# Performance work log

Measured on AMD Instinct MI355X. Metric: run time of the kernel, lower is better.

## Reference

```python
import jax, jax.numpy as jnp
import numpy as np

KS = 4                                  # kernel_size per axis
K = KS ** 3                             # 64 spatial filter bins
RADIUS = np.float32(1.5 * 6 * 0.025 / 2.0)   # filter_extent / 2 = 0.1125
N_REAL = 20000                          # fluid particles (index N_REAL = far dummy)
E_PAD = 1200000                         # padded edge count


def ball_to_cube(u):
    # volume-preserving unit-ball -> [-1,1]^3 cube map (Griepentrog et al., as in
    # Open3D-ML 'ball_to_cube_volume_preserving'): ball -> cylinder -> cube.
    eps = 1e-9
    x, y, z = u[..., 0], u[..., 1], u[..., 2]
    sq = x * x + y * y + z * z
    norm = jnp.sqrt(sq + eps)
    rxy2 = x * x + y * y
    polar = 1.25 * z * z > rxy2          # top/bottom cone region
    s = jnp.where(polar,
                  jnp.sqrt(3.0 * norm / (norm + jnp.abs(z) + eps)),
                  norm / jnp.sqrt(rxy2 + eps))
    xc = x * s
    yc = y * s
    zc = jnp.where(polar, jnp.sign(z) * norm, 1.5 * z)
    degen = sq < 1e-12
    xc = jnp.where(degen, 0.0, xc)
    yc = jnp.where(degen, 0.0, yc)
    zc = jnp.where(degen, 0.0, zc)
    # cylinder -> cube: inverse concentric (Shirley-Chiu) area-preserving map on xy
    r = jnp.sqrt(xc * xc + yc * yc + eps)
    c1 = jnp.abs(xc) >= jnp.abs(yc)
    xs = jnp.where(jnp.abs(xc) < eps, eps, xc)
    ys = jnp.where(jnp.abs(yc) < eps, eps, yc)
    fop = np.float32(4.0 / np.pi)
    a = jnp.where(c1, jnp.sign(xc) * r, jnp.sign(yc) * r * fop * jnp.arctan(xc / ys))
    b = jnp.where(c1, jnp.sign(xc) * r * fop * jnp.arctan(yc / xs), jnp.sign(yc) * r)
    tiny = (xc * xc + yc * yc) < 1e-12
    a = jnp.where(tiny, 0.0, a)
    b = jnp.where(tiny, 0.0, b)
    return jnp.stack([a, b, zc], axis=-1)


def cconv(feat, pos, src, dst, W, b):
    # ContinuousConv: normalize=False, align_corners=True, linear interpolation,
    # poly6 window on r^2/radius^2, self-neighbors excluded in the edge list.
    offs = (pos[dst] - pos[src]) / RADIUS              # (E,3), inside unit ball
    r2 = jnp.sum(offs * offs, axis=-1)
    win = jnp.clip((1.0 - r2) ** 3, 0.0, 1.0)          # window_poly6; 0 on pad edges
    g = jnp.clip((ball_to_cube(offs) * 0.5 + 0.5) * (KS - 1), 0.0, KS - 1)
    f0f = jnp.floor(g)
    t = g - f0f                                         # trilinear fractions
    f0 = f0f.astype(jnp.int32)
    fj = feat[dst] * win[:, None]                       # (E,Cin) windowed neighbor feats
    n = pos.shape[0]
    cin = feat.shape[1]
    B = jnp.zeros((n * K, cin), feat.dtype)             # per-query per-bin accumulator
    for c in range(8):                                  # 8 trilinear corners
        w = jnp.ones_like(r2)
        kf = jnp.zeros_like(src)
        for ax in range(3):
            bit = (c >> (2 - ax)) & 1
            ia = jnp.minimum(f0[:, ax] + bit, KS - 1)
            w = w * (t[:, ax] if bit else 1.0 - t[:, ax])
            kf = kf * KS + ia
        B = B + jax.ops.segment_sum(fj * w[:, None], src * K + kf, num_segments=n * K)
    out = jnp.einsum('nki,kio->no', B.reshape(n, K, cin), W.reshape(K, cin, -1))
    return out + b


def forward(pos, feats, edge_src, edge_dst, conv0_w, conv0_b, dense0_w, dense0_b,
            conv1_w, conv1_b, dense1_w, dense1_b, conv2_w, conv2_b, dense2_w, dense2_b,
            conv3_w, conv3_b, dense3_w, dense3_b):
    f = jnp.concatenate([jnp.ones_like(pos[:, :1]), feats], axis=-1)   # 13 channels
    x = jnp.concatenate([cconv(f, pos, edge_src, edge_dst, conv0_w, conv0_b),
                         f @ dense0_w + dense0_b], axis=-1)            # 64 + 32 = 96
    layers = [(conv1_w, conv1_b, dense1_w, dense1_b),
              (conv2_w, conv2_b, dense2_w, dense2_b),
              (conv3_w, conv3_b, dense3_w, dense3_b)]
    for cw, cb, dw, db in layers:
        inp = jax.nn.relu(x)
        y = cconv(inp, pos, edge_src, edge_dst, cw, cb) + inp @ dw + db
        x = (y + x) if y.shape[-1] == x.shape[-1] else y               # residual 64->64
    return (x * (1.0 / 128.0))[:N_REAL]                                # pos_correction


def setup_inputs() -> dict:
    rng = np.random.default_rng(0)
    spacing = 0.05                                  # 2 * particle_radius
    g = np.arange(28)
    pts = np.stack(np.meshgrid(g, g, g, indexing='ij'), -1).reshape(-1, 3).astype(np.float64) * spacing
    pts = pts[:N_REAL] + rng.uniform(-0.012, 0.012, (N_REAL, 3))
    # fixed-radius neighbor search, excluding self (radius_search_ignore_query_points)
    r2 = float(RADIUS) ** 2
    sq = (pts ** 2).sum(-1)
    src_l, dst_l = [], []
    for s in range(0, N_REAL, 1000):
        q = pts[s:s + 1000]
        d2 = (q ** 2).sum(-1)[:, None] + sq[None, :] - 2.0 * (q @ pts.T)
        ii, jj = np.nonzero(d2 < r2)
        ii = ii + s
        keep = ii != jj
        src_l.append(ii[keep])
        dst_l.append(jj[keep])
    src = np.concatenate(src_l).astype(np.int32)[:E_PAD]
    dst = np.concatenate(dst_l).astype(np.int32)[:E_PAD]
    pad = E_PAD - src.size
    src = np.concatenate([src, np.zeros(pad, np.int32)])
    dst = np.concatenate([dst, np.full(pad, N_REAL, np.int32)])   # edges to far dummy -> window 0
    pos = np.concatenate([pts, [[1e3, 1e3, 1e3]]], 0).astype(np.float32)
    key = jax.random.key(0)
    ks = jax.random.split(key, 12)
    def w(k, shape, fan_in):
        return jax.random.normal(k, shape, jnp.float32) * np.float32(1.0 / np.sqrt(fan_in))
    return {
        'pos': jnp.asarray(pos),
        'feats': jax.random.normal(ks[0], (N_REAL + 1, 12), jnp.float32),
        'edge_src': jnp.asarray(src),
        'edge_dst': jnp.asarray(dst),
        'conv0_w': w(ks[1], (KS, KS, KS, 13, 64), 13 * 27),
        'conv0_b': jnp.zeros((64,), jnp.float32),
        'dense0_w': w(ks[2], (13, 32), 13),
        'dense0_b': jnp.zeros((32,), jnp.float32),
        'conv1_w': w(ks[3], (KS, KS, KS, 96, 64), 96 * 27),
        'conv1_b': jnp.zeros((64,), jnp.float32),
        'dense1_w': w(ks[4], (96, 64), 96),
        'dense1_b': jnp.zeros((64,), jnp.float32),
        'conv2_w': w(ks[5], (KS, KS, KS, 64, 64), 64 * 27),
        'conv2_b': jnp.zeros((64,), jnp.float32),
        'dense2_w': w(ks[6], (64, 64), 64),
        'dense2_b': jnp.zeros((64,), jnp.float32),
        'conv3_w': w(ks[7], (KS, KS, KS, 64, 3), 64 * 27),
        'conv3_b': jnp.zeros((3,), jnp.float32),
        'dense3_w': w(ks[8], (64, 3), 64),
        'dense3_b': jnp.zeros((3,), jnp.float32),
    }


def reference(pos, feats, edge_src, edge_dst, conv0_w, conv0_b, dense0_w, dense0_b,
              conv1_w, conv1_b, dense1_w, dense1_b, conv2_w, conv2_b, dense2_w, dense2_b,
              conv3_w, conv3_b, dense3_w, dense3_b):
    return forward(pos, feats, edge_src, edge_dst, conv0_w, conv0_b, dense0_w, dense0_b,
                   conv1_w, conv1_b, dense1_w, dense1_b, conv2_w, conv2_b, dense2_w, dense2_b,
                   conv3_w, conv3_b, dense3_w, dense3_b)
```

## Files before the change

kernel.cpp:

```cpp
#include <hip/hip_runtime.h>
#include <math.h>

#define NPTS   20001
#define NREAL  20000
#define EPAD   1200000
#define KK     64
#define RADF   0.1125f

typedef _Float16 half8_t __attribute__((ext_vector_type(8)));
typedef float    floatx4 __attribute__((ext_vector_type(4)));

__device__ __forceinline__ float sgnf(float v){ return v>0.f ? 1.f : (v<0.f ? -1.f : 0.f); }
__device__ __forceinline__ _Float16 lo16(unsigned u){ return __builtin_bit_cast(_Float16, (unsigned short)(u & 0xffffu)); }
__device__ __forceinline__ _Float16 hi16(unsigned u){ return __builtin_bit_cast(_Float16, (unsigned short)(u >> 16)); }

__device__ __forceinline__ void* swzp(void* base, int byteoff){
  return (void*)((char*)base + (byteoff ^ (((byteoff >> 6) & 7) << 4)));
}
__device__ __forceinline__ const void* swzp(const void* base, int byteoff){
  return (const void*)((const char*)base + (byteoff ^ (((byteoff >> 6) & 7) << 4)));
}

__global__ void k_find_ereal(const int* __restrict__ dst, int* __restrict__ ereal){
  int lo=0, hi=EPAD;
  while(lo<hi){ int mid=(lo+hi)>>1; if(dst[mid]==NREAL) hi=mid; else lo=mid+1; }
  *ereal = lo;
}

__global__ void k_csr(const int* __restrict__ src, const int* __restrict__ erealp,
                      int* __restrict__ row_start){
  int i = blockIdx.x*blockDim.x + threadIdx.x;
  if(i > NPTS) return;
  int E = *erealp;
  int lo=0, hi=E;
  while(lo<hi){ int mid=(lo+hi)>>1; if(src[mid] < i) lo=mid+1; else hi=mid; }
  row_start[i] = lo;
}

__global__ void k_build_f(const float* __restrict__ feats, float* __restrict__ f){
  int idx = blockIdx.x*blockDim.x + threadIdx.x;
  if(idx >= NPTS*13) return;
  int i = idx/13, c = idx - i*13;
  f[idx] = (c==0) ? 1.f : feats[i*12 + (c-1)];
}

__global__ void k_cvtF(const float* __restrict__ x, unsigned* __restrict__ Fp, int total){
  int idx = blockIdx.x*blockDim.x + threadIdx.x;
  if(idx >= total) return;
  float v = fmaxf(x[idx], 0.f);
  _Float16 h = (_Float16)v;
  _Float16 l = (_Float16)(v - (float)h);
  Fp[idx] = (unsigned)__builtin_bit_cast(unsigned short, h)
          | ((unsigned)__builtin_bit_cast(unsigned short, l) << 16);
}

__device__ __forceinline__ void edge_geom(float ox, float oy, float oz,
                                          float& win, float& t0, float& t1, float& t2, int& f0p){
  const float eps = 1e-9f;
  float sq = ox*ox + oy*oy + oz*oz;
  float u = 1.f - sq;
  win = fminf(fmaxf(u*u*u, 0.f), 1.f);
  float norm = sqrtf(sq + eps);
  float rxy2 = ox*ox + oy*oy;
  bool polar = (1.25f*oz*oz > rxy2);
  float s_p = sqrtf(3.f*norm/(norm + fabsf(oz) + eps));
  float s_n = norm / sqrtf(rxy2 + eps);
  float s = polar ? s_p : s_n;
  float xc = ox*s, yc = oy*s;
  float zc = polar ? sgnf(oz)*norm : 1.5f*oz;
  if(sq < 1e-12f){ xc = 0.f; yc = 0.f; zc = 0.f; }
  float r = sqrtf(xc*xc + yc*yc + eps);
  bool c1 = fabsf(xc) >= fabsf(yc);
  float xs = (fabsf(xc) < eps) ? eps : xc;
  float ys = (fabsf(yc) < eps) ? eps : yc;
  const float fop = 1.2732395447351628f;
  float a = c1 ? sgnf(xc)*r : sgnf(yc)*r*fop*atanf(xc/ys);
  float b = c1 ? sgnf(xc)*r*fop*atanf(yc/xs) : sgnf(yc)*r;
  if(xc*xc + yc*yc < 1e-12f){ a = 0.f; b = 0.f; }
  float g0 = fminf(fmaxf((a *0.5f+0.5f)*3.f, 0.f), 3.f);
  float g1 = fminf(fmaxf((b *0.5f+0.5f)*3.f, 0.f), 3.f);
  float g2 = fminf(fmaxf((zc*0.5f+0.5f)*3.f, 0.f), 3.f);
  float f00 = floorf(g0), f01 = floorf(g1), f02 = floorf(g2);
  t0 = g0 - f00; t1 = g1 - f01; t2 = g2 - f02;
  f0p = (int)f00 | ((int)f01 << 2) | ((int)f02 << 4);
}

__global__ __launch_bounds__(256) void k_geom(const float* __restrict__ pos,
    const int* __restrict__ esrc, const int* __restrict__ edst,
    float4* __restrict__ gw, int4* __restrict__ gmz)
{
  int e = blockIdx.x*blockDim.x + threadIdx.x;
  if(e >= EPAD) return;
  const int sn = esrc[e], d = edst[e];
  const float ox = (pos[d*3+0]-pos[sn*3+0])/RADF;
  const float oy = (pos[d*3+1]-pos[sn*3+1])/RADF;
  const float oz = (pos[d*3+2]-pos[sn*3+2])/RADF;
  float win, t0, t1, t2; int f0p;
  edge_geom(ox, oy, oz, win, t0, t1, t2, f0p);
  const int i0 = f0p & 3, i1 = (f0p>>2) & 3, i2 = f0p >> 4;
  const int X0 = i0 << 4, X1 = ((i0+1)&3) << 4;
  const int Y0 = i1 << 2, Y1 = ((i1+1)&3) << 2;
  const int Z0 = i2, Z1 = (i2+1) & 3;
  const float wx0 = win*(1.f-t0), wx1 = win*t0;
  const float wy0 = 1.f-t1, wy1 = t1;
  const float wz0 = 1.f-t2, wz1 = t2;
  gw[e] = make_float4(wx0*wy0, wx0*wy1, wx1*wy0, wx1*wy1);
  const int p0 = Z0 & 1;
  const float zA = p0 ? wz1 : wz0;
  const int   cA = p0 ? Z1 : Z0;
  const int   cB = p0 ? Z0 : Z1;
  const int cells0 = (X0|Y0|cA) | ((X0|Y1|cA)<<8) | ((X1|Y0|cA)<<16) | ((X1|Y1|cA)<<24);
  const int cells1 = (X0|Y0|cB) | ((X0|Y1|cB)<<8) | ((X1|Y0|cB)<<16) | ((X1|Y1|cB)<<24);
  gmz[e] = make_int4(__float_as_int(zA), cells0, cells1, d);
}

template<int OUT3>
__global__ __launch_bounds__(256) void k_scat64m(
    const unsigned* __restrict__ Fp, const float4* __restrict__ gw,
    const int4* __restrict__ gmz, const int* __restrict__ row_start,
    float* __restrict__ B, int node_base,
    const float* __restrict__ W3, float* __restrict__ out)
{
  __shared__ __align__(128) _Float16 Wh[64*32];
  __shared__ __align__(128) _Float16 Wl[64*32];
  __shared__ __align__(128) _Float16 Fh[64*32];
  __shared__ __align__(128) _Float16 Fl[64*32];
  __shared__ __align__(16) float4 Sq[32];
  __shared__ __align__(16) int4   Smd[32];
  __shared__ float red[16];

  const int tid  = threadIdx.x;
  const int node = node_base + blockIdx.x;
  const int wv   = tid >> 6;
  const int lane = tid & 63;
  const int frow = lane & 15;
  const int fb   = (lane >> 4) << 4;

  floatx4 acc[4];
  #pragma unroll
  for(int nt=0;nt<4;++nt){ acc[nt][0]=0.f; acc[nt][1]=0.f; acc[nt][2]=0.f; acc[nt][3]=0.f; }

  half8_t hz;
  #pragma unroll
  for(int q8=0;q8<8;++q8) hz[q8] = (_Float16)0;

  const int e0 = row_start[node], e1 = row_start[node+1];

  for(int eb = e0; eb < e1; eb += 32){
    const int n = (e1 - eb < 32) ? (e1 - eb) : 32;
    __syncthreads();
    if(wv == 0){
      if(lane < 32){
        int ei = eb + lane; if(ei >= e1) ei = e1 - 1;
        Sq[lane]  = gw[ei];
        Smd[lane] = gmz[ei];
      }
    } else {
      for(int j = tid - 64; j < 512; j += 192){
        if(j < 256) ((half8_t*)Wh)[j]       = hz;
        else        ((half8_t*)Wl)[j - 256] = hz;
      }
    }
    __syncthreads();
    {
      half8_t hreg, lreg;
      #pragma unroll
      for(int j=0;j<8;++j){
        const int dst = Smd[wv*8 + j].w;
        const unsigned u = Fp[(size_t)dst*64 + lane];
        hreg[j] = lo16(u);
        lreg[j] = hi16(u);
      }
      *(half8_t*)swzp(Fh, (lane<<6) + (wv<<4)) = hreg;
      *(half8_t*)swzp(Fl, (lane<<6) + (wv<<4)) = lreg;
    }
    if(lane < 8){
      const int ei = wv*8 + lane;
      if(ei < n){
        const float4 q  = Sq[ei];
        const int4   md = Smd[ei];
        const float zA = __int_as_float(md.x), zB = 1.f - zA;
        #pragma unroll
        for(int t=0;t<8;++t){
          const int   cells = (t < 4) ? md.y : md.z;
          const float zz    = (t < 4) ? zA : zB;
          const int   cell  = (cells >> ((t & 3) * 8)) & 255;
          const float qq    = ((t&3)==0) ? q.x : ((t&3)==1) ? q.y : ((t&3)==2) ? q.z : q.w;
          const float wgt   = qq * zz;
          const _Float16 h  = (_Float16)wgt;
          *(_Float16*)swzp(Wh, (cell<<6) + (ei<<1)) = h;
          *(_Float16*)swzp(Wl, (cell<<6) + (ei<<1)) = (_Float16)(wgt - (float)h);
        }
      }
    }
    __syncthreads();
    const half8_t ah = *(const half8_t*)swzp(Wh, ((wv*16 + frow)<<6) + fb);
    const half8_t al = *(const half8_t*)swzp(Wl, ((wv*16 + frow)<<6) + fb);
    #pragma unroll
    for(int nt=0; nt<4; ++nt){
      const half8_t bh = *(const half8_t*)swzp(Fh, ((nt*16 + frow)<<6) + fb);
      const half8_t bl = *(const half8_t*)swzp(Fl, ((nt*16 + frow)<<6) + fb);
      acc[nt] = __builtin_amdgcn_mfma_f32_16x16x32_f16(ah, bh, acc[nt], 0, 0, 0);
      acc[nt] = __builtin_amdgcn_mfma_f32_16x16x32_f16(al, bh, acc[nt], 0, 0, 0);
      acc[nt] = __builtin_amdgcn_mfma_f32_16x16x32_f16(ah, bl, acc[nt], 0, 0, 0);
    }
  }

  if(!OUT3){
    float* Bg = B + (size_t)blockIdx.x*4096;
    #pragma unroll
    for(int nt=0;nt<4;++nt)
      #pragma unroll
      for(int r=0;r<4;++r){
        const int cell = wv*16 + (lane>>4)*4 + r;
        Bg[cell*64 + nt*16 + (lane&15)] = acc[nt][r];
      }
  } else {
    float s0=0.f, s1=0.f, s2=0.f;
    #pragma unroll
    for(int nt=0;nt<4;++nt){
      #pragma unroll
      for(int r=0;r<4;++r){
        const int cell = wv*16 + (lane>>4)*4 + r;
        const int j3   = (cell*64 + nt*16 + (lane&15)) * 3;
        const float v  = acc[nt][r];
        s0 = fmaf(v, W3[j3+0], s0);
        s1 = fmaf(v, W3[j3+1], s1);
        s2 = fmaf(v, W3[j3+2], s2);
      }
    }
    #pragma unroll
    for(int off = 32; off > 0; off >>= 1){
      s0 += __shfl_down(s0, off);
      s1 += __shfl_down(s1, off);
      s2 += __shfl_down(s2, off);
    }
    if(lane == 0){
      red[wv*4+0] = s0; red[wv*4+1] = s1; red[wv*4+2] = s2;
    }
    __syncthreads();
    if(tid == 0 && node < NREAL){
      out[node*3+0] += (red[0]+red[4]+red[8] +red[12])*(1.f/128.f);
      out[node*3+1] += (red[1]+red[5]+red[9] +red[13])*(1.f/128.f);
      out[node*3+2] += (red[2]+red[6]+red[10]+red[14])*(1.f/128.f);
    }
  }
}

__global__ __launch_bounds__(256) void k_scat96m(
    const unsigned* __restrict__ Fp, const float4* __restrict__ gw,
    const int4* __restrict__ gmz, const int* __restrict__ row_start,
    float* __restrict__ B, int node_base)
{
  __shared__ __align__(128) _Float16 Wh[64*32];
  __shared__ __align__(128) _Float16 Wl[64*32];
  __shared__ __align__(128) _Float16 Fh[96*32];
  __shared__ __align__(128) _Float16 Fl[96*32];
  __shared__ __align__(16) float4 Sq[32];
  __shared__ __align__(16) int4   Smd[32];

  const int tid  = threadIdx.x;
  const int node = node_base + blockIdx.x;
  const int wv   = tid >> 6;
  const int lane = tid & 63;
  const int frow = lane & 15;
  const int fb   = (lane >> 4) << 4;

  floatx4 acc[6];
  #pragma unroll
  for(int nt=0;nt<6;++nt){ acc[nt][0]=0.f; acc[nt][1]=0.f; acc[nt][2]=0.f; acc[nt][3]=0.f; }

  half8_t hz;
  #pragma unroll
  for(int q8=0;q8<8;++q8) hz[q8] = (_Float16)0;

  const int e0 = row_start[node], e1 = row_start[node+1];

  for(int eb = e0; eb < e1; eb += 32){
    const int n = (e1 - eb < 32) ? (e1 - eb) : 32;
    __syncthreads();
    if(wv == 0){
      if(lane < 32){
        int ei = eb + lane; if(ei >= e1) ei = e1 - 1;
        Sq[lane]  = gw[ei];
        Smd[lane] = gmz[ei];
      }
    } else {
      for(int j = tid - 64; j < 512; j += 192){
        if(j < 256) ((half8_t*)Wh)[j]       = hz;
        else        ((half8_t*)Wl)[j - 256] = hz;
      }
    }
    __syncthreads();
    {
      half8_t h0, l0, h1, l1;
      #pragma unroll
      for(int j=0;j<8;++j){
        const int dst = Smd[wv*8 + j].w;
        const unsigned u = Fp[(size_t)dst*96 + lane];
        h0[j] = lo16(u);
        l0[j] = hi16(u);
        if(lane < 32){
          const unsigned u2 = Fp[(size_t)dst*96 + 64 + lane];
          h1[j] = lo16(u2);
          l1[j] = hi16(u2);
        }
      }
      *(half8_t*)swzp(Fh, (lane<<6) + (wv<<4)) = h0;
      *(half8_t*)swzp(Fl, (lane<<6) + (wv<<4)) = l0;
      if(lane < 32){
        *(half8_t*)swzp(Fh, ((64+lane)<<6) + (wv<<4)) = h1;
        *(half8_t*)swzp(Fl, ((64+lane)<<6) + (wv<<4)) = l1;
      }
    }
    if(lane < 8){
      const int ei = wv*8 + lane;
      if(ei < n){
        const float4 q  = Sq[ei];
        const int4   md = Smd[ei];
        const float zA = __int_as_float(md.x), zB = 1.f - zA;
        #pragma unroll
        for(int t=0;t<8;++t){
          const int   cells = (t < 4) ? md.y : md.z;
          const float zz    = (t < 4) ? zA : zB;
          const int   cell  = (cells >> ((t & 3) * 8)) & 255;
          const float qq    = ((t&3)==0) ? q.x : ((t&3)==1) ? q.y : ((t&3)==2) ? q.z : q.w;
          const float wgt   = qq * zz;
          const _Float16 h  = (_Float16)wgt;
          *(_Float16*)swzp(Wh, (cell<<6) + (ei<<1)) = h;
          *(_Float16*)swzp(Wl, (cell<<6) + (ei<<1)) = (_Float16)(wgt - (float)h);
        }
      }
    }
    __syncthreads();
    const half8_t ah = *(const half8_t*)swzp(Wh, ((wv*16 + frow)<<6) + fb);
    const half8_t al = *(const half8_t*)swzp(Wl, ((wv*16 + frow)<<6) + fb);
    #pragma unroll
    for(int nt=0; nt<6; ++nt){
      const half8_t bh = *(const half8_t*)swzp(Fh, ((nt*16 + frow)<<6) + fb);
      const half8_t bl = *(const half8_t*)swzp(Fl, ((nt*16 + frow)<<6) + fb);
      acc[nt] = __builtin_amdgcn_mfma_f32_16x16x32_f16(ah, bh, acc[nt], 0, 0, 0);
      acc[nt] = __builtin_amdgcn_mfma_f32_16x16x32_f16(al, bh, acc[nt], 0, 0, 0);
      acc[nt] = __builtin_amdgcn_mfma_f32_16x16x32_f16(ah, bl, acc[nt], 0, 0, 0);
    }
  }

  float* Bg = B + (size_t)blockIdx.x*6144;
  #pragma unroll
  for(int nt=0;nt<6;++nt)
    #pragma unroll
    for(int r=0;r<4;++r){
      const int cell = wv*16 + (lane>>4)*4 + r;
      Bg[cell*96 + nt*16 + (lane&15)] = acc[nt][r];
    }
}

__global__ __launch_bounds__(128) void k_scat13(
    const float* __restrict__ feat, const float4* __restrict__ gw,
    const int4* __restrict__ gmz, const int* __restrict__ row_start,
    float* __restrict__ B, int node_base)
{
  constexpr int CIN = 13, BSZ = KK*CIN, ESW = 4, CSTRIDE = BSZ + 8;
  __shared__ __align__(16) float Bl[ESW*CSTRIDE];
  const int tid  = threadIdx.x;
  const int node = node_base + blockIdx.x;

  for(int j = tid; j < ESW*CSTRIDE; j += 128) Bl[j] = 0.f;

  const int e0 = row_start[node], e1 = row_start[node+1];
  const int wv   = tid >> 6;
  const int lane = tid & 63;
  const int slot = lane >> 4;
  const int c    = lane & 15;
  const bool act = (c < CIN);
  float* Bp = Bl + slot*CSTRIDE;
  __syncthreads();

  if(act){
    for(int e = e0 + slot; e < e1; e += ESW){
      const float4 q  = gw[e];
      const int4   md = gmz[e];
      const float zA = __int_as_float(md.x);
      const float z  = wv ? (1.f - zA) : zA;
      const int   cp = wv ? md.z : md.y;
      float v = feat[(size_t)md.w*CIN + c] * z;
      const int b0 = ( cp        & 255)*CIN + c;
      const int b1 = ((cp >> 8)  & 255)*CIN + c;
      const int b2 = ((cp >> 16) & 255)*CIN + c;
      const int b3 = (((unsigned)cp) >> 24)*CIN + c;
      float o0 = Bp[b0], o1 = Bp[b1], o2 = Bp[b2], o3 = Bp[b3];
      o0 = fmaf(q.x, v, o0); o1 = fmaf(q.y, v, o1);
      o2 = fmaf(q.z, v, o2); o3 = fmaf(q.w, v, o3);
      Bp[b0] = o0; Bp[b1] = o1; Bp[b2] = o2; Bp[b3] = o3;
    }
  }
  __syncthreads();

  float* Bg = B + (size_t)blockIdx.x*BSZ;
  for(int j = tid*4; j < BSZ; j += 512){
    float4 a = *(const float4*)&Bl[j];
    #pragma unroll
    for(int k = 1; k < ESW; ++k){
      const float4 t = *(const float4*)&Bl[k*CSTRIDE + j];
      a.x += t.x; a.y += t.y; a.z += t.z; a.w += t.w;
    }
    *(float4*)&Bg[j] = a;
  }
}

__global__ void k_cvtW(const float* __restrict__ W, _Float16* __restrict__ WhT,
                       _Float16* __restrict__ WlT, int Kd)
{
  int idx = blockIdx.x*blockDim.x + threadIdx.x;
  if(idx >= 64*Kd) return;
  int o = idx / Kd, k = idx - o*Kd;
  float w = W[(size_t)k*64 + o];
  _Float16 h = (_Float16)w;
  WhT[idx] = h;
  WlT[idx] = (_Float16)(w - (float)h);
}

__global__ __launch_bounds__(256) void k_gemm_mfma(
    const float* __restrict__ A, const _Float16* __restrict__ WhT,
    const _Float16* __restrict__ WlT, float* __restrict__ P,
    int M, int Kd, int node_base, int ksteps_per)
{
  __shared__ __align__(128) _Float16 Ah[64*32];
  __shared__ __align__(128) _Float16 Al[64*32];
  __shared__ __align__(128) _Float16 Bh[64*32];
  __shared__ __align__(128) _Float16 Blo[64*32];
  const int tid = threadIdx.x;
  const int mbase = blockIdx.x * 64;
  const int s = blockIdx.y;
  const int kt0 = s * ksteps_per * 32;
  const int kt1 = min(Kd, kt0 + ksteps_per*32);
  const int wv = tid >> 6, lane = tid & 63;
  const int row  = tid >> 2;
  const int kseg = (tid & 3) * 8;
  const int sb   = (tid & 3) << 4;
  const int frow = lane & 15;
  const int fb   = (lane >> 4) << 4;

  floatx4 acc[4];
  #pragma unroll
  for(int c=0;c<4;++c){ acc[c][0]=0.f; acc[c][1]=0.f; acc[c][2]=0.f; acc[c][3]=0.f; }

  const int grow = mbase + row;
  const float* Arow = (grow < M) ? (A + (size_t)grow*Kd) : nullptr;
  const _Float16* WhRow = WhT + (size_t)row*Kd;
  const _Float16* WlRow = WlT + (size_t)row*Kd;

  for(int kt = kt0; kt < kt1; kt += 32){
    float av[8];
    if(Arow){
      *(float4*)&av[0] = *(const float4*)(Arow + kt + kseg);
      *(float4*)&av[4] = *(const float4*)(Arow + kt + kseg + 4);
    } else {
      #pragma unroll
      for(int j=0;j<8;++j) av[j] = 0.f;
    }
    half8_t hv, lv;
    #pragma unroll
    for(int j=0;j<8;++j){
      _Float16 h = (_Float16)av[j];
      hv[j] = h;
      lv[j] = (_Float16)(av[j] - (float)h);
    }
    half8_t wh = *(const half8_t*)(WhRow + kt + kseg);
    half8_t wl = *(const half8_t*)(WlRow + kt + kseg);
    __syncthreads();
    *(half8_t*)swzp(Ah,  (row<<6) + sb) = hv;
    *(half8_t*)swzp(Al,  (row<<6) + sb) = lv;
    *(half8_t*)swzp(Bh,  (row<<6) + sb) = wh;
    *(half8_t*)swzp(Blo, (row<<6) + sb) = wl;
    __syncthreads();
    const half8_t ah = *(const half8_t*)swzp(Ah, ((wv*16 + frow)<<6) + fb);
    const half8_t al = *(const half8_t*)swzp(Al, ((wv*16 + frow)<<6) + fb);
    #pragma unroll
    for(int c=0;c<4;++c){
      const half8_t bh = *(const half8_t*)swzp(Bh,  ((c*16 + frow)<<6) + fb);
      const half8_t bl = *(const half8_t*)swzp(Blo, ((c*16 + frow)<<6) + fb);
      acc[c] = __builtin_amdgcn_mfma_f32_16x16x32_f16(ah, bh, acc[c], 0, 0, 0);
      acc[c] = __builtin_amdgcn_mfma_f32_16x16x32_f16(al, bh, acc[c], 0, 0, 0);
      acc[c] = __builtin_amdgcn_mfma_f32_16x16x32_f16(ah, bl, acc[c], 0, 0, 0);
    }
  }

  const int prow0 = mbase + wv*16 + (lane>>4)*4;
  const int pcol  = lane & 15;
  #pragma unroll
  for(int c=0;c<4;++c){
    #pragma unroll
    for(int r=0;r<4;++r){
      const int rr = prow0 + r;
      if(rr < M)
        P[((size_t)s*NPTS + node_base + rr)*64 + c*16 + pcol] = acc[c][r];
    }
  }
}

template<int S>
__global__ void k_combine(const float* __restrict__ P, float* __restrict__ x,
                          int ldout, int colofs)
{
  int idx = blockIdx.x*blockDim.x + threadIdx.x;
  if(idx >= NPTS*16) return;
  int node = idx >> 4, c4 = (idx & 15) * 4;
  float4 s = *(const float4*)(P + (size_t)node*64 + c4);
  #pragma unroll
  for(int k=1;k<S;++k){
    float4 t = *(const float4*)(P + ((size_t)k*NPTS + node)*64 + c4);
    s.x+=t.x; s.y+=t.y; s.z+=t.z; s.w+=t.w;
  }
  float* xp = x + (size_t)node*ldout + colofs + c4;
  float4 o = *(float4*)xp;
  o.x+=s.x; o.y+=s.y; o.z+=s.z; o.w+=s.w;
  *(float4*)xp = o;
}

__global__ void k_dense0(const float* __restrict__ f, const float* __restrict__ dW,
                         const float* __restrict__ db, const float* __restrict__ cb0,
                         float* __restrict__ out)
{
  int idx = blockIdx.x*blockDim.x + threadIdx.x;
  if(idx >= NPTS*96) return;
  int i = idx/96, c = idx - i*96;
  if(c < 64){ out[idx] = cb0[c]; return; }
  int o = c - 64;
  float s = db[o];
  const float* row = f + (size_t)i*13;
  #pragma unroll
  for(int j=0;j<13;++j) s = fmaf(row[j], dW[j*32+o], s);
  out[idx] = s;
}

__global__ void k_dense(const float* __restrict__ in, int cin,
                        const float* __restrict__ dW, const float* __restrict__ db,
                        const float* __restrict__ cb, const float* __restrict__ resid,
                        float* __restrict__ out)
{
  int idx = blockIdx.x*blockDim.x + threadIdx.x;
  if(idx >= NPTS*64) return;
  int i = idx >> 6, o = idx & 63;
  float s = db[o] + cb[o];
  if(resid) s += resid[idx];
  const float* row = in + (size_t)i*cin;
  for(int c=0;c<cin;++c) s = fmaf(fmaxf(row[c],0.f), dW[c*64+o], s);
  out[idx] = s;
}

__global__ void k_dense3(const float* __restrict__ x2, const float* __restrict__ dW,
                         const float* __restrict__ db, const float* __restrict__ cb,
                         float* __restrict__ out)
{
  int idx = blockIdx.x*blockDim.x + threadIdx.x;
  if(idx >= NREAL*3) return;
  int i = idx/3, o = idx - i*3;
  float s = db[o] + cb[o];
  const float* row = x2 + (size_t)i*64;
  for(int c=0;c<64;++c) s = fmaf(fmaxf(row[c],0.f), dW[c*3+o], s);
  out[idx] = s * (1.f/128.f);
}

static inline size_t alup(size_t x){ return (x + 255) & ~(size_t)255; }

static inline int calc_rows(size_t bcap, int cin, int want){
  size_t perrow = (size_t)KK * cin * 4;
  size_t r = (perrow > 0) ? bcap / perrow : 0;
  if(r >= (size_t)want) return want;
  r = (r / 128) * 128;
  if(r < 128) r = 128;
  return (int)r;
}

extern "C" void kernel_launch(void* const* d_in, const int* in_sizes, int n_in,
                              void* d_out, int out_size, void* d_ws, size_t ws_size,
                              hipStream_t stream)
{
  const float* pos   = (const float*)d_in[0];
  const float* feats = (const float*)d_in[1];
  const int*   esrc  = (const int*)d_in[2];
  const int*   edst  = (const int*)d_in[3];
  const float* c0w = (const float*)d_in[4];
  const float* c0b = (const float*)d_in[5];
  const float* d0w = (const float*)d_in[6];
  const float* d0b = (const float*)d_in[7];
  const float* c1w = (const float*)d_in[8];
  const float* c1b = (const float*)d_in[9];
  const float* d1w = (const float*)d_in[10];
  const float* d1b = (const float*)d_in[11];
  const float* c2w = (const float*)d_in[12];
  const float* c2b = (const float*)d_in[13];
  const float* d2w = (const float*)d_in[14];
  const float* d2b = (const float*)d_in[15];
  const float* c3w = (const float*)d_in[16];
  const float* c3b = (const float*)d_in[17];
  const float* d3w = (const float*)d_in[18];
  const float* d3b = (const float*)d_in[19];
  float* out = (float*)d_out;

  char* w = (char*)d_ws;
  size_t off = 0;
  float* f  = (float*)(w+off); off += alup((size_t)NPTS*13*4);
  float* x0 = (float*)(w+off); off += alup((size_t)NPTS*96*4);
  float* x1 = (float*)(w+off); off += alup((size_t)NPTS*64*4);
  float* x2 = (float*)(w+off); off += alup((size_t)NPTS*64*4);
  int* row_start = (int*)(w+off); off += alup((size_t)(NPTS+1)*4);
  int* ereal = (int*)(w+off);     off += alup(16);
  float4* gw = (float4*)(w+off);  off += alup((size_t)EPAD*16);
  int4*  gmz = (int4*)(w+off);    off += alup((size_t)EPAD*16);
  float* P  = (float*)(w+off); off += alup((size_t)8*NPTS*64*4);
  _Float16* whT = (_Float16*)(w+off); off += alup((size_t)64*6144*2);
  _Float16* wlT = (_Float16*)(w+off); off += alup((size_t)64*6144*2);
  unsigned* Fp0 = (unsigned*)(w+off); off += alup((size_t)NPTS*96*4);
  unsigned* Fp1 = (unsigned*)(w+off); off += alup((size_t)NPTS*64*4);
  float* B = (float*)(w+off);
  size_t bcap = (ws_size > off) ? (ws_size - off) : 0;

  k_find_ereal<<<1,1,0,stream>>>(edst, ereal);
  k_csr<<<(NPTS+1+255)/256,256,0,stream>>>(esrc, ereal, row_start);
  k_build_f<<<(NPTS*13+255)/256,256,0,stream>>>(feats, f);
  k_geom<<<(EPAD+255)/256,256,0,stream>>>(pos, esrc, edst, gw, gmz);

  k_dense0<<<(NPTS*96+255)/256,256,0,stream>>>(f, d0w, d0b, c0b, x0);
  {
    k_cvtW<<<(64*832+255)/256,256,0,stream>>>(c0w, whT, wlT, 832);
    int rows = calc_rows(bcap, 13, 8192);
    for(int base = 0; base < NPTS; base += rows){
      int m = (NPTS - base < rows) ? (NPTS - base) : rows;
      k_scat13<<<m,128,0,stream>>>(f, gw, gmz, row_start, B, base);
      k_gemm_mfma<<<dim3((m+63)/64, 8),256,0,stream>>>(B, whT, wlT, P, m, 832, base, 4);
    }
    k_combine<8><<<(NPTS*16+255)/256,256,0,stream>>>(P, x0, 96, 0);
  }

  k_dense<<<(NPTS*64+255)/256,256,0,stream>>>(x0, 96, d1w, d1b, c1b, nullptr, x1);
  {
    k_cvtW<<<(64*6144+255)/256,256,0,stream>>>(c1w, whT, wlT, 6144);
    k_cvtF<<<(NPTS*96+255)/256,256,0,stream>>>(x0, Fp0, NPTS*96);
    int rows = calc_rows(bcap, 96, 4096);
    for(int base = 0; base < NPTS; base += rows){
      int m = (NPTS - base < rows) ? (NPTS - base) : rows;
      k_scat96m<<<m,256,0,stream>>>(Fp0, gw, gmz, row_start, B, base);
      k_gemm_mfma<<<dim3((m+63)/64, 8),256,0,stream>>>(B, whT, wlT, P, m, 6144, base, 24);
    }
    k_combine<8><<<(NPTS*16+255)/256,256,0,stream>>>(P, x1, 64, 0);
  }

  k_dense<<<(NPTS*64+255)/256,256,0,stream>>>(x1, 64, d2w, d2b, c2b, x1, x2);
  {
    k_cvtW<<<(64*4096+255)/256,256,0,stream>>>(c2w, whT, wlT, 4096);
    k_cvtF<<<(NPTS*64+255)/256,256,0,stream>>>(x1, Fp1, NPTS*64);
    int rows = calc_rows(bcap, 64, 4096);
    for(int base = 0; base < NPTS; base += rows){
      int m = (NPTS - base < rows) ? (NPTS - base) : rows;
      k_scat64m<0><<<m,256,0,stream>>>(Fp1, gw, gmz, row_start, B, base, nullptr, nullptr);
      k_gemm_mfma<<<dim3((m+63)/64, 8),256,0,stream>>>(B, whT, wlT, P, m, 4096, base, 16);
    }
    k_combine<8><<<(NPTS*16+255)/256,256,0,stream>>>(P, x2, 64, 0);
  }

  k_dense3<<<(NREAL*3+255)/256,256,0,stream>>>(x2, d3w, d3b, c3b, out);
  k_cvtF<<<(NPTS*64+255)/256,256,0,stream>>>(x2, Fp1, NPTS*64);
  k_scat64m<1><<<NPTS,256,0,stream>>>(Fp1, gw, gmz, row_start, nullptr, 0, c3w, out);
}
```

Before: 968.5 us.

## Pre-split scatter output into packed fp16 hi/lo and enlarge GEMM M-tile

The scatter kernels now write their per-node basis matrix B as packed fp16 hi/lo pairs instead of fp32, so the GEMM no longer does the split-conversion per tile. The GEMM block tile grows from 64 to 128 rows, with each wave computing two 16-row tiles, so every weight tile loaded into shared memory is reused across twice as many rows. B traffic stays the same size (4 bytes per element) but conversion work moves to the producer. The larger tile halves the grid in M and raises register use from the accumulators, which may lower occupancy.

```diff
diff --git a/kernel.cpp b/kernel.cpp
--- a/kernel.cpp
+++ b/kernel.cpp
@@ -13,6 +13,12 @@
 __device__ __forceinline__ float sgnf(float v){ return v>0.f ? 1.f : (v<0.f ? -1.f : 0.f); }
 __device__ __forceinline__ _Float16 lo16(unsigned u){ return __builtin_bit_cast(_Float16, (unsigned short)(u & 0xffffu)); }
 __device__ __forceinline__ _Float16 hi16(unsigned u){ return __builtin_bit_cast(_Float16, (unsigned short)(u >> 16)); }
+__device__ __forceinline__ unsigned packf(float v){
+  _Float16 h = (_Float16)v;
+  _Float16 l = (_Float16)(v - (float)h);
+  return (unsigned)__builtin_bit_cast(unsigned short, h)
+       | ((unsigned)__builtin_bit_cast(unsigned short, l) << 16);
+}
 
 __device__ __forceinline__ void* swzp(void* base, int byteoff){
   return (void*)((char*)base + (byteoff ^ (((byteoff >> 6) & 7) << 4)));
@@ -47,11 +53,7 @@
 __global__ void k_cvtF(const float* __restrict__ x, unsigned* __restrict__ Fp, int total){
   int idx = blockIdx.x*blockDim.x + threadIdx.x;
   if(idx >= total) return;
-  float v = fmaxf(x[idx], 0.f);
-  _Float16 h = (_Float16)v;
-  _Float16 l = (_Float16)(v - (float)h);
-  Fp[idx] = (unsigned)__builtin_bit_cast(unsigned short, h)
-          | ((unsigned)__builtin_bit_cast(unsigned short, l) << 16);
+  Fp[idx] = packf(fmaxf(x[idx], 0.f));
 }
 
 __device__ __forceinline__ void edge_geom(float ox, float oy, float oz,
@@ -118,7 +120,7 @@
 __global__ __launch_bounds__(256) void k_scat64m(
     const unsigned* __restrict__ Fp, const float4* __restrict__ gw,
     const int4* __restrict__ gmz, const int* __restrict__ row_start,
-    float* __restrict__ B, int node_base,
+    unsigned* __restrict__ B, int node_base,
     const float* __restrict__ W3, float* __restrict__ out)
 {
   __shared__ __align__(128) _Float16 Wh[64*32];
@@ -207,13 +209,13 @@
   }
 
   if(!OUT3){
-    float* Bg = B + (size_t)blockIdx.x*4096;
+    unsigned* Bg = B + (size_t)blockIdx.x*4096;
     #pragma unroll
     for(int nt=0;nt<4;++nt)
       #pragma unroll
       for(int r=0;r<4;++r){
         const int cell = wv*16 + (lane>>4)*4 + r;
-        Bg[cell*64 + nt*16 + (lane&15)] = acc[nt][r];
+        Bg[cell*64 + nt*16 + (lane&15)] = packf(acc[nt][r]);
       }
   } else {
     float s0=0.f, s1=0.f, s2=0.f;
@@ -250,7 +252,7 @@
 __global__ __launch_bounds__(256) void k_scat96m(
     const unsigned* __restrict__ Fp, const float4* __restrict__ gw,
     const int4* __restrict__ gmz, const int* __restrict__ row_start,
-    float* __restrict__ B, int node_base)
+    unsigned* __restrict__ B, int node_base)
 {
   __shared__ __align__(128) _Float16 Wh[64*32];
   __shared__ __align__(128) _Float16 Wl[64*32];
@@ -345,20 +347,20 @@
     }
   }
 
-  float* Bg = B + (size_t)blockIdx.x*6144;
+  unsigned* Bg = B + (size_t)blockIdx.x*6144;
   #pragma unroll
   for(int nt=0;nt<6;++nt)
     #pragma unroll
     for(int r=0;r<4;++r){
       const int cell = wv*16 + (lane>>4)*4 + r;
-      Bg[cell*96 + nt*16 + (lane&15)] = acc[nt][r];
+      Bg[cell*96 + nt*16 + (lane&15)] = packf(acc[nt][r]);
     }
 }
 
 __global__ __launch_bounds__(128) void k_scat13(
     const float* __restrict__ feat, const float4* __restrict__ gw,
     const int4* __restrict__ gmz, const int* __restrict__ row_start,
-    float* __restrict__ B, int node_base)
+    unsigned* __restrict__ B, int node_base)
 {
   constexpr int CIN = 13, BSZ = KK*CIN, ESW = 4, CSTRIDE = BSZ + 8;
   __shared__ __align__(16) float Bl[ESW*CSTRIDE];
@@ -396,7 +398,7 @@
   }
   __syncthreads();
 
-  float* Bg = B + (size_t)blockIdx.x*BSZ;
+  unsigned* Bg = B + (size_t)blockIdx.x*BSZ;
   for(int j = tid*4; j < BSZ; j += 512){
     float4 a = *(const float4*)&Bl[j];
     #pragma unroll
@@ -404,7 +406,9 @@
       const float4 t = *(const float4*)&Bl[k*CSTRIDE + j];
       a.x += t.x; a.y += t.y; a.z += t.z; a.w += t.w;
     }
-    *(float4*)&Bg[j] = a;
+    uint4 o;
+    o.x = packf(a.x); o.y = packf(a.y); o.z = packf(a.z); o.w = packf(a.w);
+    *(uint4*)&Bg[j] = o;
   }
 }
 
@@ -421,80 +425,100 @@
 }
 
 __global__ __launch_bounds__(256) void k_gemm_mfma(
-    const float* __restrict__ A, const _Float16* __restrict__ WhT,
+    const unsigned* __restrict__ Ap, const _Float16* __restrict__ WhT,
     const _Float16* __restrict__ WlT, float* __restrict__ P,
     int M, int Kd, int node_base, int ksteps_per)
 {
-  __shared__ __align__(128) _Float16 Ah[64*32];
-  __shared__ __align__(128) _Float16 Al[64*32];
+  __shared__ __align__(128) _Float16 Ah[128*32];
+  __shared__ __align__(128) _Float16 Al[128*32];
   __shared__ __align__(128) _Float16 Bh[64*32];
   __shared__ __align__(128) _Float16 Blo[64*32];
   const int tid = threadIdx.x;
-  const int mbase = blockIdx.x * 64;
+  const int mbase = blockIdx.x * 128;
   const int s = blockIdx.y;
   const int kt0 = s * ksteps_per * 32;
   const int kt1 = min(Kd, kt0 + ksteps_per*32);
   const int wv = tid >> 6, lane = tid & 63;
-  const int row  = tid >> 2;
-  const int kseg = (tid & 3) * 8;
-  const int sb   = (tid & 3) << 4;
+  const int arow = tid >> 1;
+  const int aseg = (tid & 1) * 16;
+  const int wrow = tid >> 2;
+  const int wseg = (tid & 3) * 8;
   const int frow = lane & 15;
   const int fb   = (lane >> 4) << 4;
 
-  floatx4 acc[4];
-  #pragma unroll
-  for(int c=0;c<4;++c){ acc[c][0]=0.f; acc[c][1]=0.f; acc[c][2]=0.f; acc[c][3]=0.f; }
-
-  const int grow = mbase + row;
-  const float* Arow = (grow < M) ? (A + (size_t)grow*Kd) : nullptr;
-  const _Float16* WhRow = WhT + (size_t)row*Kd;
-  const _Float16* WlRow = WlT + (size_t)row*Kd;
+  floatx4 acc[2][4];
+  #pragma unroll
+  for(int rt=0;rt<2;++rt)
+    #pragma unroll
+    for(int c=0;c<4;++c){ acc[rt][c][0]=0.f; acc[rt][c][1]=0.f; acc[rt][c][2]=0.f; acc[rt][c][3]=0.f; }
+
+  const int grow = mbase + arow;
+  const unsigned* Arow = (grow < M) ? (Ap + (size_t)grow*Kd) : nullptr;
+  const _Float16* WhRow = WhT + (size_t)wrow*Kd;
+  const _Float16* WlRow = WlT + (size_t)wrow*Kd;
 
   for(int kt = kt0; kt < kt1; kt += 32){
-    float av[8];
+    unsigned au[16];
     if(Arow){
-      *(float4*)&av[0] = *(const float4*)(Arow + kt + kseg);
-      *(float4*)&av[4] = *(const float4*)(Arow + kt + kseg + 4);
+      *(uint4*)&au[0]  = *(const uint4*)(Arow + kt + aseg);
+      *(uint4*)&au[4]  = *(const uint4*)(Arow + kt + aseg + 4);
+      *(uint4*)&au[8]  = *(const uint4*)(Arow + kt + aseg + 8);
+      *(uint4*)&au[12] = *(const uint4*)(Arow + kt + aseg + 12);
     } else {
       #pragma unroll
-      for(int j=0;j<8;++j) av[j] = 0.f;
-    }
-    half8_t hv, lv;
+      for(int j=0;j<16;++j) au[j] = 0u;
+    }
+    half8_t h0, h1, l0, l1;
     #pragma unroll
     for(int j=0;j<8;++j){
-      _Float16 h = (_Float16)av[j];
-      hv[j] = h;
-      lv[j] = (_Float16)(av[j] - (float)h);
-    }
-    half8_t wh = *(const half8_t*)(WhRow + kt + kseg);
-    half8_t wl = *(const half8_t*)(WlRow + kt + kseg);
-    __syncthreads();
-    *(half8_t*)swzp(Ah,  (row<<6) + sb) = hv;
-    *(half8_t*)swzp(Al,  (row<<6) + sb) = lv;
-    *(half8_t*)swzp(Bh,  (row<<6) + sb) = wh;
-    *(half8_t*)swzp(Blo, (row<<6) + sb) = wl;
-    __syncthreads();
-    const half8_t ah = *(const half8_t*)swzp(Ah, ((wv*16 + frow)<<6) + fb);
-    const half8_t al = *(const half8_t*)swzp(Al, ((wv*16 + frow)<<6) + fb);
+      h0[j] = lo16(au[j]);   l0[j] = hi16(au[j]);
+      h1[j] = lo16(au[8+j]); l1[j] = hi16(au[8+j]);
+    }
+    half8_t wh = *(const half8_t*)(WhRow + kt + wseg);
+    half8_t wl = *(const half8_t*)(WlRow + kt + wseg);
+    __syncthreads();
+    {
+      const int ab = (arow<<6) + (aseg<<1);
+      *(half8_t*)swzp(Ah, ab)      = h0;
+      *(half8_t*)swzp(Ah, ab + 16) = h1;
+      *(half8_t*)swzp(Al, ab)      = l0;
+      *(half8_t*)swzp(Al, ab + 16) = l1;
+      const int wb = (wrow<<6) + (wseg<<1);
+      *(half8_t*)swzp(Bh,  wb) = wh;
+      *(half8_t*)swzp(Blo, wb) = wl;
+    }
+    __syncthreads();
+    half8_t ah[2], al[2];
+    #pragma unroll
+    for(int rt=0;rt<2;++rt){
+      ah[rt] = *(const half8_t*)swzp(Ah, ((wv*32 + rt*16 + frow)<<6) + fb);
+      al[rt] = *(const half8_t*)swzp(Al, ((wv*32 + rt*16 + frow)<<6) + fb);
+    }
     #pragma unroll
     for(int c=0;c<4;++c){
       const half8_t bh = *(const half8_t*)swzp(Bh,  ((c*16 + frow)<<6) + fb);
       const half8_t bl = *(const half8_t*)swzp(Blo, ((c*16 + frow)<<6) + fb);
-      acc[c] = __builtin_amdgcn_mfma_f32_16x16x32_f16(ah, bh, acc[c], 0, 0, 0);
-      acc[c] = __builtin_amdgcn_mfma_f32_16x16x32_f16(al, bh, acc[c], 0, 0, 0);
-      acc[c] = __builtin_amdgcn_mfma_f32_16x16x32_f16(ah, bl, acc[c], 0, 0, 0);
-    }
-  }
-
-  const int prow0 = mbase + wv*16 + (lane>>4)*4;
-  const int pcol  = lane & 15;
-  #pragma unroll
-  for(int c=0;c<4;++c){
-    #pragma unroll
-    for(int r=0;r<4;++r){
-      const int rr = prow0 + r;
-      if(rr < M)
-        P[((size_t)s*NPTS + node_base + rr)*64 + c*16 + pcol] = acc[c][r];
+      #pragma unroll
+      for(int rt=0;rt<2;++rt){
+        acc[rt][c] = __builtin_amdgcn_mfma_f32_16x16x32_f16(ah[rt], bh, acc[rt][c], 0, 0, 0);
+        acc[rt][c] = __builtin_amdgcn_mfma_f32_16x16x32_f16(al[rt], bh, acc[rt][c], 0, 0, 0);
+        acc[rt][c] = __builtin_amdgcn_mfma_f32_16x16x32_f16(ah[rt], bl, acc[rt][c], 0, 0, 0);
+      }
+    }
+  }
+
+  const int pcol = lane & 15;
+  #pragma unroll
+  for(int rt=0;rt<2;++rt){
+    const int prow0 = mbase + wv*32 + rt*16 + (lane>>4)*4;
+    #pragma unroll
+    for(int c=0;c<4;++c){
+      #pragma unroll
+      for(int r=0;r<4;++r){
+        const int rr = prow0 + r;
+        if(rr < M)
+          P[((size_t)s*NPTS + node_base + rr)*64 + c*16 + pcol] = acc[rt][c][r];
+      }
     }
   }
 }
@@ -614,7 +638,7 @@
   _Float16* wlT = (_Float16*)(w+off); off += alup((size_t)64*6144*2);
   unsigned* Fp0 = (unsigned*)(w+off); off += alup((size_t)NPTS*96*4);
   unsigned* Fp1 = (unsigned*)(w+off); off += alup((size_t)NPTS*64*4);
-  float* B = (float*)(w+off);
+  unsigned* B = (unsigned*)(w+off);
   size_t bcap = (ws_size > off) ? (ws_size - off) : 0;
 
   k_find_ereal<<<1,1,0,stream>>>(edst, ereal);
@@ -629,7 +653,7 @@
     for(int base = 0; base < NPTS; base += rows){
       int m = (NPTS - base < rows) ? (NPTS - base) : rows;
       k_scat13<<<m,128,0,stream>>>(f, gw, gmz, row_start, B, base);
-      k_gemm_mfma<<<dim3((m+63)/64, 8),256,0,stream>>>(B, whT, wlT, P, m, 832, base, 4);
+      k_gemm_mfma<<<dim3((m+127)/128, 8),256,0,stream>>>(B, whT, wlT, P, m, 832, base, 4);
     }
     k_combine<8><<<(NPTS*16+255)/256,256,0,stream>>>(P, x0, 96, 0);
   }
@@ -642,7 +666,7 @@
     for(int base = 0; base < NPTS; base += rows){
       int m = (NPTS - base < rows) ? (NPTS - base) : rows;
       k_scat96m<<<m,256,0,stream>>>(Fp0, gw, gmz, row_start, B, base);
-      k_gemm_mfma<<<dim3((m+63)/64, 8),256,0,stream>>>(B, whT, wlT, P, m, 6144, base, 24);
+      k_gemm_mfma<<<dim3((m+127)/128, 8),256,0,stream>>>(B, whT, wlT, P, m, 6144, base, 24);
     }
     k_combine<8><<<(NPTS*16+255)/256,256,0,stream>>>(P, x1, 64, 0);
   }
@@ -655,7 +679,7 @@
     for(int base = 0; base < NPTS; base += rows){
       int m = (NPTS - base < rows) ? (NPTS - base) : rows;
       k_scat64m<0><<<m,256,0,stream>>>(Fp1, gw, gmz, row_start, B, base, nullptr, nullptr);
-      k_gemm_mfma<<<dim3((m+63)/64, 8),256,0,stream>>>(B, whT, wlT, P, m, 4096, base, 16);
+      k_gemm_mfma<<<dim3((m+127)/128, 8),256,0,stream>>>(B, whT, wlT, P, m, 4096, base, 16);
     }
     k_combine<8><<<(NPTS*16+255)/256,256,0,stream>>>(P, x2, 64, 0);
   }
```

Result: slower. 1.032 ms (+6.6%).
